# Performance work log

Hardware: AMD Instinct MI355X
Metric: run time of the kernel (lower is better)

The kernel has to match this reference:

```python
import jax, jax.numpy as jnp
import numpy as np

EPS = 1e-9
KERNEL = 3


def kernel_tile(x, kernel, stride):
    """im2col-style patch extraction. x: [B,H,W,...] -> [B,OH,OW,kernel*kernel,depth]."""
    B, H, W = x.shape[:3]
    depth = int(np.prod(x.shape[3:]))
    x = x.reshape(B, H, W, depth)
    OH = (H - kernel) // stride + 1
    OW = (W - kernel) // stride + 1
    patches = jnp.stack(
        [x[:, i:i + (OH - 1) * stride + 1:stride, j:j + (OW - 1) * stride + 1:stride, :]
         for i in range(kernel) for j in range(kernel)], axis=3)
    return patches  # [B,OH,OW,k*k,depth]


def em_routing(votes, i_act, beta_v, beta_a, routings):
    # votes: [B,S,S,I,O,16], i_act: [B,S,S,I], beta_*: [1,1,1,O]
    I, O = votes.shape[-3], votes.shape[-2]
    rr = jnp.full((I, O, 1), 1.0 / O, dtype=votes.dtype)
    i_act = i_act[..., None, None]           # [B,S,S,I,1,1]
    bv = beta_v[..., None, :, None]          # [1,1,1,1,O,1]
    ba = beta_a[..., None, :, None]
    it_min, it_max = 1.0, min(float(routings), 3.0)
    o_mean = o_act = None
    for it in range(routings):
        inv_temp = it_min + (it_max - it_min) * it / max(1.0, routings - 1.0)
        # M-step
        rr_prime = rr * i_act                                        # [B,S,S,I,O,1]
        rr_sum = jnp.sum(rr_prime, axis=-3, keepdims=True)           # [B,S,S,1,O,1]
        o_mean = jnp.sum(rr_prime * votes, axis=-3, keepdims=True) / rr_sum  # [B,S,S,1,O,16]
        o_stdv = jnp.sqrt(jnp.sum(rr_prime * jnp.square(votes - o_mean), axis=-3, keepdims=True) / rr_sum)
        o_cost = (bv + jnp.log(o_stdv + EPS)) * rr_sum               # [B,S,S,1,O,16]
        o_act = jax.nn.sigmoid(inv_temp * (ba - jnp.sum(o_cost, axis=-1, keepdims=True)))  # [B,S,S,1,O,1]
        if it < routings - 1:
            # E-step: log Gaussian prob of each vote under each output capsule
            o_p = (-jnp.sum(jnp.square(votes - o_mean) / (2.0 * jnp.square(o_stdv)), axis=-1, keepdims=True)
                   - jnp.sum(jnp.log(o_stdv + EPS), axis=-1, keepdims=True))  # [B,S,S,I,O,1]
            zz = jnp.log(o_act + EPS) + o_p
            rr = jax.nn.softmax(zz, axis=-2)                          # softmax over O
    pose = jnp.squeeze(o_mean, axis=-3)      # [B,S,S,O,16]
    act = jnp.squeeze(o_act, axis=(-3, -1))  # [B,S,S,O]
    return pose, act


def setup_inputs() -> dict:
    key = jax.random.key(0)
    ks = jax.random.split(key, 5)
    B, H, W, I_SIZE, O_SIZE = 4, 14, 14, 32, 32
    inputs_pose = jax.random.normal(ks[0], (B, H, W, I_SIZE, 4, 4), dtype=jnp.float32)
    inputs_activation = jax.random.uniform(ks[1], (B, H, W, I_SIZE), dtype=jnp.float32)
    w = jax.random.normal(ks[2], (1, 3 * 3 * I_SIZE, O_SIZE, 4, 4), dtype=jnp.float32)
    beta_v = 0.1 * jax.random.normal(ks[3], (1, 1, 1, O_SIZE), dtype=jnp.float32)
    beta_a = 0.1 * jax.random.normal(ks[4], (1, 1, 1, O_SIZE), dtype=jnp.float32)
    return {"inputs_pose": inputs_pose, "inputs_activation": inputs_activation,
            "w": w, "beta_v": beta_v, "beta_a": beta_a, "stride": 1, "routings": 3}


def reference(inputs_pose, inputs_activation, w, beta_v, beta_a, stride, routings):
    B = inputs_pose.shape[0]
    pose_size = inputs_pose.shape[-1]            # 4
    i_size = inputs_pose.shape[3]
    o_size = w.shape[2]
    tp = kernel_tile(inputs_pose, KERNEL, stride)        # [B,S,S,9,i*16]
    ta = kernel_tile(inputs_activation, KERNEL, stride)  # [B,S,S,9,i]
    S = ta.shape[1]
    I = KERNEL * KERNEL * i_size
    poses = tp.reshape(-1, I, pose_size, pose_size)      # [N,I,4,4], N = B*S*S
    acts = ta.reshape(B, S, S, I)
    # vote transform: per (input capsule, output capsule) 4x4 matmul
    votes = jnp.einsum('nipq,ioqr->niopr', poses, w[0])  # [N,I,O,4,4]
    votes = votes.reshape(B, S, S, I, o_size, pose_size * pose_size)
    pose, activation = em_routing(votes, acts, beta_v, beta_a, routings)
    pose = pose.reshape(B, S, S, o_size, pose_size, pose_size)
    return pose, activation
```

## Files before the change

kernel.cpp:

```cpp
#include <hip/hip_runtime.h>
#include <math.h>

namespace {

constexpr int SOUT = 12;
constexpr int OCAP = 32;
constexpr int PD   = 16;
constexpr int NI   = 288;
constexpr int SUBS = 4;
constexpr int ISUB = NI / SUBS;
constexpr int NPOS = 4 * SOUT * SOUT;
constexpr float EPSF = 1e-9f;
constexpr int CHUNK = 33 * 32;
constexpr size_t POSE_OUT = (size_t)NPOS * OCAP * PD;

#define SWZ(x, msk) __int_as_float(__builtin_amdgcn_ds_swizzle(__float_as_int(x), ((msk) << 10) | 0x1F))

__device__ __forceinline__ void loadW(const float* __restrict__ p, float (&W)[16]) {
    const float4 w0 = *reinterpret_cast<const float4*>(p);
    const float4 w1 = *reinterpret_cast<const float4*>(p + 4);
    const float4 w2 = *reinterpret_cast<const float4*>(p + 8);
    const float4 w3 = *reinterpret_cast<const float4*>(p + 12);
    W[0]=w0.x; W[1]=w0.y; W[2]=w0.z; W[3]=w0.w;
    W[4]=w1.x; W[5]=w1.y; W[6]=w1.z; W[7]=w1.w;
    W[8]=w2.x; W[9]=w2.y; W[10]=w2.z; W[11]=w2.w;
    W[12]=w3.x; W[13]=w3.y; W[14]=w3.z; W[15]=w3.w;
}

__device__ __forceinline__ void vote16(const float* __restrict__ pr, const float (&W)[16], float (&v)[16]) {
    #pragma unroll
    for (int p = 0; p < 4; ++p) {
        const float4 pv = *reinterpret_cast<const float4*>(pr + p * 4);
        #pragma unroll
        for (int r = 0; r < 4; ++r)
            v[p*4+r] = fmaf(pv.x, W[r], fmaf(pv.y, W[4+r], fmaf(pv.z, W[8+r], pv.w * W[12+r])));
    }
}

template<int SWEEP>
__global__ __launch_bounds__(256, 3)
void sweep_kernel(const float* __restrict__ pose_in,
                  const float* __restrict__ act_in,
                  const float* __restrict__ wmat,
                  const float* __restrict__ beta_v,
                  const float* __restrict__ beta_a,
                  const float* __restrict__ prev,
                  float* __restrict__ outbuf)
{
    __shared__ __align__(16) float sP[ISUB * PD];
    __shared__ float sA[ISUB];
    __shared__ float sStat[OCAP][2 * PD + 2];
    __shared__ float sBias[OCAP];
    __shared__ float sRed[4][33][33];

    const int bid = blockIdx.x;
    const int n   = bid >> 2;
    const int sub = bid & 3;
    const int b   = n / (SOUT * SOUT);
    const int yx  = n % (SOUT * SOUT);
    const int y   = yx / SOUT;
    const int x   = yx % SOUT;

    const int t    = threadIdx.x;
    const int wave = t >> 6;
    const int o    = t & 31;
    const int slot = t >> 5;
    const int half = slot & 1;

    {
        const float4* src = reinterpret_cast<const float4*>(pose_in);
        float4* dst = reinterpret_cast<float4*>(sP);
        for (int u = t; u < ISUB * 4; u += 256) {
            const int il = u >> 2;
            const int i  = sub * ISUB + il;
            const int k = i >> 5, c = i & 31;
            const int ki = k / 3, kj = k - ki * 3;
            const int cell = (b * 14 + y + ki) * 14 + (x + kj);
            dst[u] = src[(size_t)(cell * 32 + c) * 4 + (u & 3)];
        }
        if (t < ISUB) {
            const int i = sub * ISUB + t;
            const int k = i >> 5, c = i & 31;
            const int ki = k / 3, kj = k - ki * 3;
            const int cell = (b * 14 + y + ki) * 14 + (x + kj);
            sA[t] = act_in[(size_t)cell * 32 + c];
        }
    }

    if constexpr (SWEEP > 0) {
        const int oo = t >> 3, dp = t & 7, d0 = dp * 2;
        const float* base = prev + (size_t)n * (SUBS * CHUNK);
        float s0 = 0.f, S1a = 0.f, S1b = 0.f, S2a = 0.f, S2b = 0.f;
        #pragma unroll
        for (int s = 0; s < SUBS; ++s) {
            const float* c = base + s * CHUNK;
            s0  += c[32 * 32 + oo];
            S1a += c[(d0)      * 32 + oo];
            S1b += c[(d0 + 1)  * 32 + oo];
            S2a += c[(16 + d0) * 32 + oo];
            S2b += c[(17 + d0) * 32 + oo];
        }
        const float inv = 1.f / s0;
        const float m0 = S1a * inv, m1 = S1b * inv;
        const float v0 = fmaxf(fmaf(-m0, m0, S2a * inv), 0.f);
        const float v1 = fmaxf(fmaf(-m1, m1, S2b * inv), 0.f);
        const float i20 = 0.5f / fmaxf(v0, 1e-30f);
        const float i21 = 0.5f / fmaxf(v1, 1e-30f);
        float ll = __logf(sqrtf(v0) + EPSF) + __logf(sqrtf(v1) + EPSF);
        float c0 = m0 * m0 * i20 + m1 * m1 * i21;
        float2 w0; w0.x = i20; w0.y = -2.f * m0 * i20;
        *reinterpret_cast<float2*>(&sStat[oo][2 * d0])     = w0;
        float2 w1; w1.x = i21; w1.y = -2.f * m1 * i21;
        *reinterpret_cast<float2*>(&sStat[oo][2 * d0 + 2]) = w1;
        #pragma unroll
        for (int m = 1; m <= 4; m <<= 1) {
            ll += __shfl_xor(ll, m, 8);
            c0 += __shfl_xor(c0, m, 8);
        }
        if (dp == 0) {
            const float cost = s0 * fmaf(16.f, beta_v[oo], ll);
            const float oact = 1.f / (1.f + __expf(-(float)SWEEP * (beta_a[oo] - cost)));
            sBias[oo] = __logf(oact + EPSF) - ll - c0;
        }
    }
    __syncthreads();

    float bias_r = 0.f;
    float i2r[PD], ngr[PD];
    if constexpr (SWEEP > 0) {
        bias_r = sBias[o];
        #pragma unroll
        for (int d = 0; d < PD; ++d) {
            const float2 p = *reinterpret_cast<const float2*>(&sStat[o][2 * d]);
            i2r[d] = p.x; ngr[d] = p.y;
        }
    }

    float s1[PD], s2[PD];
    float s0acc = 0.f;
    #pragma unroll
    for (int d = 0; d < PD; ++d) { s1[d] = 0.f; s2[d] = 0.f; }

    const float* wbase = wmat + ((size_t)(sub * ISUB + slot) * OCAP + o) * PD;

    float WA[16], WB[16];
    loadW(wbase, WA);

#define STEP(st, Wc, Wn)                                                 \
    {                                                                    \
        if ((st) < 8) loadW(wbase + (size_t)((st) + 1) * 4096, Wn);      \
        const int il = (st) * 8 + slot;                                  \
        float v[16];                                                     \
        vote16(&sP[il * PD], Wc, v);                                     \
        const float a_i = sA[il];                                        \
        float rrp;                                                       \
        if constexpr (SWEEP == 0) {                                      \
            rrp = a_i * (1.0f / 32.0f);                                  \
        } else {                                                         \
            float ts = 0.f;                                              \
            _Pragma("unroll")                                            \
            for (int d = 0; d < PD; ++d)                                 \
                ts = fmaf(v[d], fmaf(v[d], i2r[d], ngr[d]), ts);         \
            const float zz = bias_r - ts;                                \
            float m = zz;                                                \
            m = fmaxf(m, SWZ(m, 16)); m = fmaxf(m, SWZ(m, 8));           \
            m = fmaxf(m, SWZ(m, 4));  m = fmaxf(m, SWZ(m, 2));           \
            m = fmaxf(m, SWZ(m, 1));                                     \
            const float e = __expf(zz - m);                              \
            float es = e;                                                \
            es += SWZ(es, 16); es += SWZ(es, 8); es += SWZ(es, 4);       \
            es += SWZ(es, 2);  es += SWZ(es, 1);                         \
            rrp = __fdividef(e, es) * a_i;                               \
        }                                                                \
        s0acc += rrp;                                                    \
        _Pragma("unroll")                                                \
        for (int d = 0; d < PD; ++d) {                                   \
            s1[d] = fmaf(rrp, v[d], s1[d]);                              \
            s2[d] = fmaf(rrp * v[d], v[d], s2[d]);                       \
        }                                                                \
    }

    STEP(0, WA, WB); STEP(1, WB, WA); STEP(2, WA, WB); STEP(3, WB, WA);
    STEP(4, WA, WB); STEP(5, WB, WA); STEP(6, WA, WB); STEP(7, WB, WA);
    STEP(8, WA, WB);
#undef STEP

    #pragma unroll
    for (int d = 0; d < PD; ++d) {
        s1[d] += __shfl_xor(s1[d], 32, 64);
        s2[d] += __shfl_xor(s2[d], 32, 64);
    }
    s0acc += __shfl_xor(s0acc, 32, 64);

    if (half == 0) {
        #pragma unroll
        for (int d = 0; d < PD; ++d) {
            sRed[wave][d][o]      = s1[d];
            sRed[wave][16 + d][o] = s2[d];
        }
        sRed[wave][32][o] = s0acc;
    }
    __syncthreads();

    float* dstc = outbuf + (size_t)bid * CHUNK;
    const int oc = t & 31;
    for (int j = t >> 5; j < 33; j += 8)
        dstc[j * 32 + oc] = sRed[0][j][oc] + sRed[1][j][oc] + sRed[2][j][oc] + sRed[3][j][oc];
}

__global__ __launch_bounds__(256, 4)
void final_kernel(const float* __restrict__ prev,
                  const float* __restrict__ beta_v,
                  const float* __restrict__ beta_a,
                  float* __restrict__ out)
{
    const int n  = blockIdx.x;
    const int t  = threadIdx.x;
    const int oo = t >> 3, dp = t & 7, d0 = dp * 2;
    const float* base = prev + (size_t)n * (SUBS * CHUNK);
    float s0 = 0.f, S1a = 0.f, S1b = 0.f, S2a = 0.f, S2b = 0.f;
    #pragma unroll
    for (int s = 0; s < SUBS; ++s) {
        const float* c = base + s * CHUNK;
        s0  += c[32 * 32 + oo];
        S1a += c[(d0)      * 32 + oo];
        S1b += c[(d0 + 1)  * 32 + oo];
        S2a += c[(16 + d0) * 32 + oo];
        S2b += c[(17 + d0) * 32 + oo];
    }
    const float inv = 1.f / s0;
    const float m0 = S1a * inv, m1 = S1b * inv;
    out[(size_t)n * (OCAP * PD) + oo * PD + d0]     = m0;
    out[(size_t)n * (OCAP * PD) + oo * PD + d0 + 1] = m1;

    const float v0 = fmaxf(fmaf(-m0, m0, S2a * inv), 0.f);
    const float v1 = fmaxf(fmaf(-m1, m1, S2b * inv), 0.f);
    float lt = __logf(sqrtf(v0) + EPSF) + __logf(sqrtf(v1) + EPSF);
    lt += __shfl_xor(lt, 1, 8);
    lt += __shfl_xor(lt, 2, 8);
    lt += __shfl_xor(lt, 4, 8);
    if (dp == 0) {
        const float cost = s0 * fmaf(16.f, beta_v[oo], lt);
        const float oact = 1.f / (1.f + __expf(-3.0f * (beta_a[oo] - cost)));
        out[POSE_OUT + (size_t)n * OCAP + oo] = oact;
    }
}

}

extern "C" void kernel_launch(void* const* d_in, const int* in_sizes, int n_in,
                              void* d_out, int out_size, void* d_ws, size_t ws_size,
                              hipStream_t stream) {
    const float* pose_in = (const float*)d_in[0];
    const float* act_in  = (const float*)d_in[1];
    const float* wmat    = (const float*)d_in[2];
    const float* beta_v  = (const float*)d_in[3];
    const float* beta_a  = (const float*)d_in[4];
    float* out = (float*)d_out;

    float* bufA = (float*)d_ws;
    float* bufB = bufA + (size_t)NPOS * SUBS * CHUNK;

    dim3 block(256);
    dim3 gridS(NPOS * SUBS);
    dim3 gridF(NPOS);

    sweep_kernel<0><<<gridS, block, 0, stream>>>(pose_in, act_in, wmat, beta_v, beta_a, nullptr, bufA);
    sweep_kernel<1><<<gridS, block, 0, stream>>>(pose_in, act_in, wmat, beta_v, beta_a, bufA, bufB);
    sweep_kernel<2><<<gridS, block, 0, stream>>>(pose_in, act_in, wmat, beta_v, beta_a, bufB, bufA);
    final_kernel<<<gridF, block, 0, stream>>>(bufA, beta_v, beta_a, out);
}
```

Baseline: 118.0 us.

## Vectorize sweep kernel with packed float2 FMAs and DPP reductions

Rewrites the vote transform, E-step distance and accumulation in sweep_kernel to use two-wide float vectors, so the compiler can emit packed FP32 FMA instructions. The 32-lane softmax max/sum reductions now use DPP row operations plus one swizzle instead of five ds_swizzle steps. sStat is laid out as separate i2/neg-mean halves, and shared-memory reduction space is halved by doing a two-phase accumulation with an extra barrier. Launch bounds drop from 3 to 2 blocks per SM, which gives more registers per thread but lowers occupancy.

```diff
diff --git a/kernel.cpp b/kernel.cpp
--- a/kernel.cpp
+++ b/kernel.cpp
@@ -14,31 +14,64 @@
 constexpr int CHUNK = 33 * 32;
 constexpr size_t POSE_OUT = (size_t)NPOS * OCAP * PD;
 
-#define SWZ(x, msk) __int_as_float(__builtin_amdgcn_ds_swizzle(__float_as_int(x), ((msk) << 10) | 0x1F))
-
-__device__ __forceinline__ void loadW(const float* __restrict__ p, float (&W)[16]) {
+typedef float v2f __attribute__((ext_vector_type(2)));
+
+__device__ __forceinline__ v2f vfma(v2f a, v2f b, v2f c) { return __builtin_elementwise_fma(a, b, c); }
+__device__ __forceinline__ v2f splat(float a) { v2f r; r.x = a; r.y = a; return r; }
+
+template<int CTRL>
+__device__ __forceinline__ float dppf(float x) {
+    return __int_as_float(__builtin_amdgcn_update_dpp(0, __float_as_int(x), CTRL, 0xF, 0xF, true));
+}
+#define SWZ16(x) __int_as_float(__builtin_amdgcn_ds_swizzle(__float_as_int(x), (16 << 10) | 0x1F))
+
+__device__ __forceinline__ float redmax32(float x) {
+    x = fmaxf(x, dppf<0xB1>(x));
+    x = fmaxf(x, dppf<0x4E>(x));
+    x = fmaxf(x, dppf<0x141>(x));
+    x = fmaxf(x, dppf<0x140>(x));
+    x = fmaxf(x, SWZ16(x));
+    return x;
+}
+__device__ __forceinline__ float redsum32(float x) {
+    x += dppf<0xB1>(x);
+    x += dppf<0x4E>(x);
+    x += dppf<0x141>(x);
+    x += dppf<0x140>(x);
+    x += SWZ16(x);
+    return x;
+}
+
+__device__ __forceinline__ void loadW(const float* __restrict__ p, v2f (&W)[8]) {
     const float4 w0 = *reinterpret_cast<const float4*>(p);
     const float4 w1 = *reinterpret_cast<const float4*>(p + 4);
     const float4 w2 = *reinterpret_cast<const float4*>(p + 8);
     const float4 w3 = *reinterpret_cast<const float4*>(p + 12);
-    W[0]=w0.x; W[1]=w0.y; W[2]=w0.z; W[3]=w0.w;
-    W[4]=w1.x; W[5]=w1.y; W[6]=w1.z; W[7]=w1.w;
-    W[8]=w2.x; W[9]=w2.y; W[10]=w2.z; W[11]=w2.w;
-    W[12]=w3.x; W[13]=w3.y; W[14]=w3.z; W[15]=w3.w;
-}
-
-__device__ __forceinline__ void vote16(const float* __restrict__ pr, const float (&W)[16], float (&v)[16]) {
+    W[0].x=w0.x; W[0].y=w0.y; W[1].x=w0.z; W[1].y=w0.w;
+    W[2].x=w1.x; W[2].y=w1.y; W[3].x=w1.z; W[3].y=w1.w;
+    W[4].x=w2.x; W[4].y=w2.y; W[5].x=w2.z; W[5].y=w2.w;
+    W[6].x=w3.x; W[6].y=w3.y; W[7].x=w3.z; W[7].y=w3.w;
+}
+
+__device__ __forceinline__ void vote8(const float* __restrict__ pr, const v2f (&W)[8], v2f (&v)[8]) {
     #pragma unroll
     for (int p = 0; p < 4; ++p) {
         const float4 pv = *reinterpret_cast<const float4*>(pr + p * 4);
         #pragma unroll
-        for (int r = 0; r < 4; ++r)
-            v[p*4+r] = fmaf(pv.x, W[r], fmaf(pv.y, W[4+r], fmaf(pv.z, W[8+r], pv.w * W[12+r])));
-    }
-}
+        for (int h = 0; h < 2; ++h) {
+            v2f acc = splat(pv.w) * W[6 + h];
+            acc = vfma(splat(pv.z), W[4 + h], acc);
+            acc = vfma(splat(pv.y), W[2 + h], acc);
+            acc = vfma(splat(pv.x), W[0 + h], acc);
+            v[p * 2 + h] = acc;
+        }
+    }
+}
+
+__device__ __forceinline__ constexpr int DH(int h) { return (h >> 1) * 4 + (h & 1) * 2; }
 
 template<int SWEEP>
-__global__ __launch_bounds__(256, 3)
+__global__ __launch_bounds__(256, 2)
 void sweep_kernel(const float* __restrict__ pose_in,
                   const float* __restrict__ act_in,
                   const float* __restrict__ wmat,
@@ -49,9 +82,9 @@
 {
     __shared__ __align__(16) float sP[ISUB * PD];
     __shared__ float sA[ISUB];
-    __shared__ float sStat[OCAP][2 * PD + 2];
+    __shared__ __align__(8) float sStat[OCAP][2 * PD + 2];
     __shared__ float sBias[OCAP];
-    __shared__ float sRed[4][33][33];
+    __shared__ float sRed[2][33][33];
 
     const int bid = blockIdx.x;
     const int n   = bid >> 2;
@@ -108,10 +141,10 @@
         const float i21 = 0.5f / fmaxf(v1, 1e-30f);
         float ll = __logf(sqrtf(v0) + EPSF) + __logf(sqrtf(v1) + EPSF);
         float c0 = m0 * m0 * i20 + m1 * m1 * i21;
-        float2 w0; w0.x = i20; w0.y = -2.f * m0 * i20;
-        *reinterpret_cast<float2*>(&sStat[oo][2 * d0])     = w0;
-        float2 w1; w1.x = i21; w1.y = -2.f * m1 * i21;
-        *reinterpret_cast<float2*>(&sStat[oo][2 * d0 + 2]) = w1;
+        sStat[oo][d0]          = i20;
+        sStat[oo][d0 + 1]      = i21;
+        sStat[oo][16 + d0]     = -2.f * m0 * i20;
+        sStat[oo][17 + d0]     = -2.f * m1 * i21;
         #pragma unroll
         for (int m = 1; m <= 4; m <<= 1) {
             ll += __shfl_xor(ll, m, 8);
@@ -126,58 +159,57 @@
     __syncthreads();
 
     float bias_r = 0.f;
-    float i2r[PD], ngr[PD];
+    v2f i2r[8], ngr[8];
     if constexpr (SWEEP > 0) {
         bias_r = sBias[o];
         #pragma unroll
-        for (int d = 0; d < PD; ++d) {
-            const float2 p = *reinterpret_cast<const float2*>(&sStat[o][2 * d]);
-            i2r[d] = p.x; ngr[d] = p.y;
-        }
-    }
-
-    float s1[PD], s2[PD];
+        for (int h = 0; h < 8; ++h) {
+            i2r[h] = *reinterpret_cast<const v2f*>(&sStat[o][2 * h]);
+            ngr[h] = *reinterpret_cast<const v2f*>(&sStat[o][16 + 2 * h]);
+        }
+    }
+
+    v2f s1[8], s2[8];
     float s0acc = 0.f;
     #pragma unroll
-    for (int d = 0; d < PD; ++d) { s1[d] = 0.f; s2[d] = 0.f; }
+    for (int h = 0; h < 8; ++h) { s1[h] = splat(0.f); s2[h] = splat(0.f); }
 
     const float* wbase = wmat + ((size_t)(sub * ISUB + slot) * OCAP + o) * PD;
 
-    float WA[16], WB[16];
+    v2f WA[8], WB[8];
     loadW(wbase, WA);
 
-#define STEP(st, Wc, Wn)                                                 \
-    {                                                                    \
-        if ((st) < 8) loadW(wbase + (size_t)((st) + 1) * 4096, Wn);      \
-        const int il = (st) * 8 + slot;                                  \
-        float v[16];                                                     \
-        vote16(&sP[il * PD], Wc, v);                                     \
-        const float a_i = sA[il];                                        \
-        float rrp;                                                       \
-        if constexpr (SWEEP == 0) {                                      \
-            rrp = a_i * (1.0f / 32.0f);                                  \
-        } else {                                                         \
-            float ts = 0.f;                                              \
-            _Pragma("unroll")                                            \
-            for (int d = 0; d < PD; ++d)                                 \
-                ts = fmaf(v[d], fmaf(v[d], i2r[d], ngr[d]), ts);         \
-            const float zz = bias_r - ts;                                \
-            float m = zz;                                                \
-            m = fmaxf(m, SWZ(m, 16)); m = fmaxf(m, SWZ(m, 8));           \
-            m = fmaxf(m, SWZ(m, 4));  m = fmaxf(m, SWZ(m, 2));           \
-            m = fmaxf(m, SWZ(m, 1));                                     \
-            const float e = __expf(zz - m);                              \
-            float es = e;                                                \
-            es += SWZ(es, 16); es += SWZ(es, 8); es += SWZ(es, 4);       \
-            es += SWZ(es, 2);  es += SWZ(es, 1);                         \
-            rrp = __fdividef(e, es) * a_i;                               \
-        }                                                                \
-        s0acc += rrp;                                                    \
-        _Pragma("unroll")                                                \
-        for (int d = 0; d < PD; ++d) {                                   \
-            s1[d] = fmaf(rrp, v[d], s1[d]);                              \
-            s2[d] = fmaf(rrp * v[d], v[d], s2[d]);                       \
-        }                                                                \
+#define STEP(st, Wc, Wn)                                                   \
+    {                                                                      \
+        if ((st) < 8) loadW(wbase + (size_t)((st) + 1) * 4096, Wn);        \
+        const int il = (st) * 8 + slot;                                    \
+        v2f v[8];                                                          \
+        vote8(&sP[il * PD], Wc, v);                                        \
+        const float a_i = sA[il];                                          \
+        float rrp;                                                         \
+        if constexpr (SWEEP == 0) {                                        \
+            rrp = a_i * (1.0f / 32.0f);                                    \
+        } else {                                                           \
+            v2f ts2 = splat(0.f);                                          \
+            _Pragma("unroll")                                              \
+            for (int h = 0; h < 8; ++h) {                                  \
+                const v2f tmp = vfma(v[h], i2r[h], ngr[h]);                \
+                ts2 = vfma(v[h], tmp, ts2);                                \
+            }                                                              \
+            const float zz = bias_r - (ts2.x + ts2.y);                     \
+            const float m = redmax32(zz);                                  \
+            const float e = __expf(zz - m);                                \
+            const float es = redsum32(e);                                  \
+            rrp = __fdividef(e, es) * a_i;                                 \
+        }                                                                  \
+        s0acc += rrp;                                                      \
+        const v2f rr2 = splat(rrp);                                        \
+        _Pragma("unroll")                                                  \
+        for (int h = 0; h < 8; ++h) {                                      \
+            const v2f rv = rr2 * v[h];                                     \
+            s1[h] = s1[h] + rv;                                            \
+            s2[h] = vfma(rv, v[h], s2[h]);                                 \
+        }                                                                  \
     }
 
     STEP(0, WA, WB); STEP(1, WB, WA); STEP(2, WA, WB); STEP(3, WB, WA);
@@ -186,26 +218,41 @@
 #undef STEP
 
     #pragma unroll
-    for (int d = 0; d < PD; ++d) {
-        s1[d] += __shfl_xor(s1[d], 32, 64);
-        s2[d] += __shfl_xor(s2[d], 32, 64);
+    for (int h = 0; h < 8; ++h) {
+        s1[h].x += __shfl_xor(s1[h].x, 32, 64);
+        s1[h].y += __shfl_xor(s1[h].y, 32, 64);
+        s2[h].x += __shfl_xor(s2[h].x, 32, 64);
+        s2[h].y += __shfl_xor(s2[h].y, 32, 64);
     }
     s0acc += __shfl_xor(s0acc, 32, 64);
 
-    if (half == 0) {
-        #pragma unroll
-        for (int d = 0; d < PD; ++d) {
-            sRed[wave][d][o]      = s1[d];
-            sRed[wave][16 + d][o] = s2[d];
+    if (wave < 2 && half == 0) {
+        #pragma unroll
+        for (int h = 0; h < 8; ++h) {
+            sRed[wave][DH(h)][o]          = s1[h].x;
+            sRed[wave][DH(h) + 1][o]      = s1[h].y;
+            sRed[wave][16 + DH(h)][o]     = s2[h].x;
+            sRed[wave][16 + DH(h) + 1][o] = s2[h].y;
         }
         sRed[wave][32][o] = s0acc;
+    }
+    __syncthreads();
+    if (wave >= 2 && half == 0) {
+        #pragma unroll
+        for (int h = 0; h < 8; ++h) {
+            sRed[wave - 2][DH(h)][o]          += s1[h].x;
+            sRed[wave - 2][DH(h) + 1][o]      += s1[h].y;
+            sRed[wave - 2][16 + DH(h)][o]     += s2[h].x;
+            sRed[wave - 2][16 + DH(h) + 1][o] += s2[h].y;
+        }
+        sRed[wave - 2][32][o] += s0acc;
     }
     __syncthreads();
 
     float* dstc = outbuf + (size_t)bid * CHUNK;
     const int oc = t & 31;
     for (int j = t >> 5; j < 33; j += 8)
-        dstc[j * 32 + oc] = sRed[0][j][oc] + sRed[1][j][oc] + sRed[2][j][oc] + sRed[3][j][oc];
+        dstc[j * 32 + oc] = sRed[0][j][oc] + sRed[1][j][oc];
 }
 
 __global__ __launch_bounds__(256, 4)
```

After: 117.7 us. Within noise of the previous version (-0.3%).
